# Performance work log

Measured on AMD Instinct MI355X. Metric: run time of the kernel, lower is better.

## Reference

```python
import jax, jax.numpy as jnp
import numpy as np

EMBED_DIM = 1024
NUM_HEADS = 16
HEAD_DIM = EMBED_DIM // NUM_HEADS


def setup_inputs() -> dict:
    key = jax.random.key(0)
    k1, k2, k3 = jax.random.split(key, 3)
    B, S = 2, 2048
    scale_in = 1.0 / np.sqrt(EMBED_DIM)
    x = jax.random.normal(k1, (B, S, EMBED_DIM), dtype=jnp.float32)
    Wqkv = jax.random.normal(k2, (EMBED_DIM, 3 * EMBED_DIM), dtype=jnp.float32) * scale_in
    bqkv = jnp.zeros((3 * EMBED_DIM,), dtype=jnp.float32)
    Wout = jax.random.normal(k3, (EMBED_DIM, EMBED_DIM), dtype=jnp.float32) * scale_in
    bout = jnp.zeros((EMBED_DIM,), dtype=jnp.float32)
    return {"x": x, "Wqkv": Wqkv, "bqkv": bqkv, "Wout": Wout, "bout": bout}


def reference(x, Wqkv, bqkv, Wout, bout):
    # Causal multi-head self-attention (dropout in eval mode = identity).
    B, S, E = x.shape
    qkv = x @ Wqkv + bqkv                                  # [B,S,3E]
    qkv = qkv.reshape(B, S, 3, NUM_HEADS, HEAD_DIM)
    qkv = jnp.transpose(qkv, (2, 0, 3, 1, 4))              # [3,B,H,S,D]
    q, k, v = qkv[0], qkv[1], qkv[2]
    scores = jnp.einsum("bhqd,bhkd->bhqk", q, k) / np.sqrt(HEAD_DIM)
    causal = jnp.tril(jnp.ones((S, S), dtype=bool))
    scores = jnp.where(causal, scores, -jnp.inf)
    attn = jax.nn.softmax(scores, axis=-1)                 # [B,H,S,S]
    out = jnp.einsum("bhqk,bhkd->bhqd", attn, v)           # [B,H,S,D]
    out = jnp.transpose(out, (0, 2, 1, 3)).reshape(B, S, E)
    return out @ Wout + bout
```

## Files before the change

### kernel.cpp

```cpp
#include <hip/hip_runtime.h>
#include <hip/hip_bf16.h>

#define BB 2
#define SS 2048
#define EE 1024
#define HH 16
#define DD 64
#define MT (BB*SS)
#define NQ (3*EE)

typedef unsigned short u16;
typedef __bf16 bf16t;
typedef bf16t bf16x8 __attribute__((ext_vector_type(8)));
typedef short short8v __attribute__((ext_vector_type(8)));
typedef float f32x4 __attribute__((ext_vector_type(4)));

#define AS1 __attribute__((address_space(1)))
#define AS3 __attribute__((address_space(3)))

__device__ __forceinline__ u16 f2b(float f) {
  unsigned u = __builtin_bit_cast(unsigned, f);
  u += 0x7FFF + ((u >> 16) & 1);
  return (u16)(u >> 16);
}

__device__ __forceinline__ unsigned cvtpk(float lo, float hi) {
  unsigned r;
  asm("v_cvt_pk_bf16_f32 %0, %1, %2" : "=v"(r) : "v"(lo), "v"(hi));
  return r;
}

__device__ __forceinline__ void gload_lds16(const void* g, void* l) {
  __builtin_amdgcn_global_load_lds((const AS1 void*)(g), (AS3 void*)(l), 16, 0, 0);
}

__device__ __forceinline__ f32x4 mfma_bf16(short8v a, short8v b, f32x4 c) {
  return __builtin_amdgcn_mfma_f32_16x16x32_bf16(
      __builtin_bit_cast(bf16x8, a), __builtin_bit_cast(bf16x8, b), c, 0, 0, 0);
}

#define QSCALE 0.18033688f

__global__ void __launch_bounds__(256) cast_kernel(const float* __restrict__ in,
                                                   u16* __restrict__ out, int n) {
  int i = (blockIdx.x * 256 + threadIdx.x) * 4;
  if (i + 3 < n) {
    float4 v = *(const float4*)(in + i);
    ushort4 o;
    o.x = f2b(v.x); o.y = f2b(v.y); o.z = f2b(v.z); o.w = f2b(v.w);
    *(ushort4*)(out + i) = o;
  }
}

__global__ void __launch_bounds__(256) transpose_kernel(const float* __restrict__ W,
                                                        u16* __restrict__ WT,
                                                        int K, int N) {
  __shared__ float t[64][65];
  int k0 = blockIdx.y * 64, n0 = blockIdx.x * 64;
  int r = threadIdx.x >> 4;
  int c4 = (threadIdx.x & 15) * 4;
#pragma unroll
  for (int i = 0; i < 4; ++i) {
    float4 v = *(const float4*)(W + (size_t)(k0 + r + i * 16) * N + n0 + c4);
    t[r + i * 16][c4 + 0] = v.x; t[r + i * 16][c4 + 1] = v.y;
    t[r + i * 16][c4 + 2] = v.z; t[r + i * 16][c4 + 3] = v.w;
  }
  __syncthreads();
#pragma unroll
  for (int i = 0; i < 4; ++i) {
    ushort4 o;
    o.x = f2b(t[c4 + 0][r + i * 16]); o.y = f2b(t[c4 + 1][r + i * 16]);
    o.z = f2b(t[c4 + 2][r + i * 16]); o.w = f2b(t[c4 + 3][r + i * 16]);
    *(ushort4*)(WT + (size_t)(n0 + r + i * 16) * K + k0 + c4) = o;
  }
}

__global__ void __launch_bounds__(256) gemm_qkv_kernel(
    const u16* __restrict__ A, const u16* __restrict__ BT,
    const float* __restrict__ bias,
    u16* __restrict__ Qs, u16* __restrict__ Ks, u16* __restrict__ Vt) {
  __shared__ u16 As[8192];
  __shared__ u16 Bs[8192];
  const int K = EE;
  int tid = threadIdx.x;
  int w = tid >> 6, lane = tid & 63;
  int g = lane >> 4, q = lane & 15;
  int m0 = blockIdx.y * 128, n0 = blockIdx.x * 128;
  int wm = (w >> 1) * 64, wn = (w & 1) * 64;

  f32x4 acc[4][4] = {};

  int r = tid >> 2;
  int kc = (tid & 3) * 8;
  const u16* ga = A + (size_t)(m0 + r) * K + kc;
  const u16* gb = BT + (size_t)(n0 + r) * K + kc;
  u16* lA0 = As + w * 512;
  u16* lA1 = As + 2048 + w * 512;
  u16* lB0 = Bs + w * 512;
  u16* lB1 = Bs + 2048 + w * 512;

  gload_lds16(ga, lA0);
  gload_lds16(ga + 64 * K, lA1);
  gload_lds16(gb, lB0);
  gload_lds16(gb + 64 * K, lB1);
  ga += 32; gb += 32;
  __syncthreads();

  int cur = 0;
  for (int k0 = 0; k0 < K; k0 += 32) {
    if (k0 + 32 < K) {
      int nx = (cur ^ 1) * 4096;
      gload_lds16(ga, lA0 + nx);
      gload_lds16(ga + 64 * K, lA1 + nx);
      gload_lds16(gb, lB0 + nx);
      gload_lds16(gb + 64 * K, lB1 + nx);
      ga += 32; gb += 32;
    }
    const u16* Ab = As + cur * 4096;
    const u16* Bb = Bs + cur * 4096;
    short8v af[4], bfv[4];
#pragma unroll
    for (int m = 0; m < 4; ++m)
      af[m] = *(const short8v*)(Ab + (wm + m * 16 + q) * 32 + g * 8);
#pragma unroll
    for (int n = 0; n < 4; ++n)
      bfv[n] = *(const short8v*)(Bb + (wn + n * 16 + q) * 32 + g * 8);
#pragma unroll
    for (int m = 0; m < 4; ++m)
#pragma unroll
      for (int n = 0; n < 4; ++n)
        acc[m][n] = mfma_bf16(af[m], bfv[n], acc[m][n]);
    __syncthreads();
    cur ^= 1;
  }

#pragma unroll
  for (int m = 0; m < 4; ++m) {
    int row0 = m0 + wm + m * 16 + g * 4;
#pragma unroll
    for (int n = 0; n < 4; ++n) {
      int col = n0 + wn + n * 16 + q;
      float bi = bias[col];
      int t = col >> 10;
      int h = (col >> 6) & 15;
      int d = col & 63;
      int b = row0 >> 11, s0 = row0 & 2047;
      size_t bh = (size_t)b * HH + h;
      if (t == 2) {
        ushort4 vv;
        vv.x = f2b(acc[m][n][0] + bi); vv.y = f2b(acc[m][n][1] + bi);
        vv.z = f2b(acc[m][n][2] + bi); vv.w = f2b(acc[m][n][3] + bi);
        *(ushort4*)&Vt[(bh * DD + d) * SS + s0] = vv;
      } else if (t == 0) {
#pragma unroll
        for (int r2 = 0; r2 < 4; ++r2)
          Qs[(bh * SS + s0 + r2) * DD + d] = f2b((acc[m][n][r2] + bi) * QSCALE);
      } else {
#pragma unroll
        for (int r2 = 0; r2 < 4; ++r2)
          Ks[(bh * SS + s0 + r2) * DD + d] = f2b(acc[m][n][r2] + bi);
      }
    }
  }
}

__global__ void __launch_bounds__(1024) attn_kernel(
    const u16* __restrict__ Qg, const u16* __restrict__ Kg,
    const u16* __restrict__ Vg, u16* __restrict__ O) {
  __shared__ char lds[132096];
  const int tid = threadIdx.x;
  const int w = tid >> 6, lane = tid & 63;
  const int hv = w >> 3, ws = w & 7;
  const int g = lane >> 4, q = lane & 15;
  const int bid = blockIdx.x;
  const int bh = bid & 31;
  const int p = 15 - (bid >> 5);
  const int b = bh >> 4, h = bh & 15;
  char* Pw = lds + 98304 + w * 2048;
  const int qsw = (q & 7) << 4;

  const char* Qp = (const char*)Qg + (size_t)bh * (SS * 128);
  const char* Kp = (const char*)Kg + (size_t)bh * (SS * 128);
  const char* Vp = (const char*)Vg + (size_t)bh * (SS * 128);

  const int tl = tid & 511;
  const int srow = tl >> 3;
  const int ssw = ((tl & 7) * 16) ^ ((srow & 7) << 4);
  const char* Ksrc = Kp + srow * 128 + ssw;
  const char* Vsrc = Vp + (size_t)srow * (SS * 2) + ssw;
  char* Kdst = lds + hv * 24576 + ws * 1024;
  char* Vdst = lds + 49152 + hv * 24576 + ws * 1024;

  const int hl = p + 1;
  const int s0 = hv * hl, send = s0 + hl;
  const int qw = p * 128 + ws * 16;

  short8v aq0 = *(const short8v*)(Qp + (size_t)(qw + q) * 128 + g * 16);
  short8v aq1 = *(const short8v*)(Qp + (size_t)(qw + q) * 128 + 64 + g * 16);

  f32x4 oacc[4] = {};
  float mrun = -1e30f, lrun = 0.f;

  gload_lds16(Ksrc + (size_t)s0 * 8192, Kdst);
  gload_lds16(Vsrc + s0 * 128, Vdst);
  if (hl > 1) {
    gload_lds16(Ksrc + (size_t)(s0 + 1) * 8192, Kdst + 8192);
    gload_lds16(Vsrc + (s0 + 1) * 128, Vdst + 8192);
  }

  for (int s = s0; s < send; ++s) {
    const int buf = (s - s0) % 3;
    if (s + 1 < send) asm volatile("s_waitcnt vmcnt(2)" ::: "memory");
    else              asm volatile("s_waitcnt vmcnt(0)" ::: "memory");
    __builtin_amdgcn_s_barrier();
    if (s + 2 < send) {
      int nb = (s + 2 - s0) % 3;
      gload_lds16(Ksrc + (size_t)(s + 2) * 8192, Kdst + nb * 8192);
      gload_lds16(Vsrc + (s + 2) * 128, Vdst + nb * 8192);
    }
    const int kv0 = s << 6;
    if (kv0 <= qw + 15) {
      const char* Kc = lds + hv * 24576 + buf * 8192;
      const char* Vc = lds + 49152 + hv * 24576 + buf * 8192;
      short8v kf[4][2];
#pragma unroll
      for (int cc = 0; cc < 4; ++cc) {
        const char* kb = Kc + (cc * 16 + q) * 128;
        kf[cc][0] = *(const short8v*)(kb + ((g * 16) ^ qsw));
        kf[cc][1] = *(const short8v*)(kb + ((64 + g * 16) ^ qsw));
      }
      f32x4 st[4];
      __builtin_amdgcn_s_setprio(1);
#pragma unroll
      for (int cc = 0; cc < 4; ++cc) {
        f32x4 z = {};
        z = mfma_bf16(kf[cc][0], aq0, z);
        z = mfma_bf16(kf[cc][1], aq1, z);
        st[cc] = z;
      }
      __builtin_amdgcn_s_setprio(0);
      short8v vf[4][2];
#pragma unroll
      for (int v = 0; v < 4; ++v) {
        const char* vb = Vc + (v * 16 + q) * 128;
        vf[v][0] = *(const short8v*)(vb + ((g * 16) ^ qsw));
        vf[v][1] = *(const short8v*)(vb + ((64 + g * 16) ^ qsw));
      }
      if (kv0 + 63 > qw) {
        int row = qw + q;
#pragma unroll
        for (int cc = 0; cc < 4; ++cc) {
          int kvb = kv0 + cc * 16 + g * 4;
#pragma unroll
          for (int r2 = 0; r2 < 4; ++r2)
            if (kvb + r2 > row) st[cc][r2] = -1e30f;
        }
      }
      f32x4 t01, t23;
#pragma unroll
      for (int r2 = 0; r2 < 4; ++r2) {
        t01[r2] = fmaxf(st[0][r2], st[1][r2]);
        t23[r2] = fmaxf(st[2][r2], st[3][r2]);
      }
      float mx = fmaxf(fmaxf(fmaxf(t01[0], t01[1]), fmaxf(t01[2], t01[3])),
                       fmaxf(fmaxf(t23[0], t23[1]), fmaxf(t23[2], t23[3])));
      mx = fmaxf(mx, __shfl_xor(mx, 16));
      mx = fmaxf(mx, __shfl_xor(mx, 32));
      if (!__all(mx - mrun <= 8.f)) {
        float mnew = fmaxf(mrun, mx);
        float alpha = exp2f(mrun - mnew);
        mrun = mnew;
        lrun *= alpha;
#pragma unroll
        for (int vfi = 0; vfi < 4; ++vfi)
#pragma unroll
          for (int r2 = 0; r2 < 4; ++r2) oacc[vfi][r2] *= alpha;
      }
      f32x4 sum4 = {};
#pragma unroll
      for (int cc = 0; cc < 4; ++cc)
#pragma unroll
        for (int r2 = 0; r2 < 4; ++r2) {
          float pv = exp2f(st[cc][r2] - mrun);
          st[cc][r2] = pv;
          sum4[r2] += pv;
        }
      float sm = (sum4[0] + sum4[1]) + (sum4[2] + sum4[3]);
      sm += __shfl_xor(sm, 16);
      sm += __shfl_xor(sm, 32);
      lrun += sm;
      char* basep = Pw + q * 128;
#pragma unroll
      for (int cc = 0; cc < 4; ++cc) {
        unsigned p01 = cvtpk(st[cc][0], st[cc][1]);
        unsigned p23 = cvtpk(st[cc][2], st[cc][3]);
        *(unsigned*)(basep + ((32 * cc + 8 * g + 0) ^ qsw)) = p01;
        *(unsigned*)(basep + ((32 * cc + 8 * g + 4) ^ qsw)) = p23;
      }
      short8v pa0 = *(const short8v*)(basep + ((g * 16) ^ qsw));
      short8v pa1 = *(const short8v*)(basep + ((64 + g * 16) ^ qsw));
      __builtin_amdgcn_s_setprio(1);
#pragma unroll
      for (int vfi = 0; vfi < 4; ++vfi) {
        oacc[vfi] = mfma_bf16(vf[vfi][0], pa0, oacc[vfi]);
        oacc[vfi] = mfma_bf16(vf[vfi][1], pa1, oacc[vfi]);
      }
      __builtin_amdgcn_s_setprio(0);
    }
  }

  __syncthreads();
  if (hv) {
    char* ob = lds + 98304 + ws * 4096;
#pragma unroll
    for (int vfi = 0; vfi < 4; ++vfi)
      *(f32x4*)(ob + vfi * 1024 + lane * 16) = oacc[vfi];
    if (g == 0)
      *(float2*)(lds + 131072 + (ws * 16 + q) * 8) = make_float2(mrun, lrun);
  }
  __syncthreads();
  if (!hv) {
    float2 ml = *(const float2*)(lds + 131072 + (ws * 16 + q) * 8);
    float mf = fmaxf(mrun, ml.x);
    float a0 = exp2f(mrun - mf);
    float a1 = exp2f(ml.x - mf);
    float inv = 1.0f / (a0 * lrun + a1 * ml.y);
    a0 *= inv; a1 *= inv;
    const char* ob = lds + 98304 + ws * 4096;
    int row = qw + q;
    char* obase = (char*)O + (((size_t)b * SS + row) * EE + h * 64) * 2;
#pragma unroll
    for (int vfi = 0; vfi < 4; ++vfi) {
      f32x4 o1 = *(const f32x4*)(ob + vfi * 1024 + lane * 16);
      uint2 o;
      o.x = cvtpk(a0 * oacc[vfi][0] + a1 * o1[0],
                  a0 * oacc[vfi][1] + a1 * o1[1]);
      o.y = cvtpk(a0 * oacc[vfi][2] + a1 * o1[2],
                  a0 * oacc[vfi][3] + a1 * o1[3]);
      *(uint2*)(obase + (vfi * 16 + g * 4) * 2) = o;
    }
  }
}

__global__ void __launch_bounds__(256) gemm_out_kernel(
    const u16* __restrict__ A, const u16* __restrict__ BT,
    const float* __restrict__ bias, float* __restrict__ Cout) {
  __shared__ u16 As[8192];
  __shared__ u16 Bs[8192];
  const int K = EE;
  int tid = threadIdx.x;
  int w = tid >> 6, lane = tid & 63;
  int g = lane >> 4, q = lane & 15;
  int m0 = blockIdx.y * 128, n0 = blockIdx.x * 128;
  int wm = (w >> 1) * 64, wn = (w & 1) * 64;

  f32x4 acc[4][4] = {};

  int r = tid >> 2;
  int kc = (tid & 3) * 8;
  const u16* ga = A + (size_t)(m0 + r) * K + kc;
  const u16* gb = BT + (size_t)(n0 + r) * K + kc;
  u16* lA0 = As + w * 512;
  u16* lA1 = As + 2048 + w * 512;
  u16* lB0 = Bs + w * 512;
  u16* lB1 = Bs + 2048 + w * 512;

  gload_lds16(ga, lA0);
  gload_lds16(ga + 64 * K, lA1);
  gload_lds16(gb, lB0);
  gload_lds16(gb + 64 * K, lB1);
  ga += 32; gb += 32;
  __syncthreads();

  int cur = 0;
  for (int k0 = 0; k0 < K; k0 += 32) {
    if (k0 + 32 < K) {
      int nx = (cur ^ 1) * 4096;
      gload_lds16(ga, lA0 + nx);
      gload_lds16(ga + 64 * K, lA1 + nx);
      gload_lds16(gb, lB0 + nx);
      gload_lds16(gb + 64 * K, lB1 + nx);
      ga += 32; gb += 32;
    }
    const u16* Ab = As + cur * 4096;
    const u16* Bb = Bs + cur * 4096;
    short8v af[4], bfv[4];
#pragma unroll
    for (int m = 0; m < 4; ++m)
      af[m] = *(const short8v*)(Ab + (wm + m * 16 + q) * 32 + g * 8);
#pragma unroll
    for (int n = 0; n < 4; ++n)
      bfv[n] = *(const short8v*)(Bb + (wn + n * 16 + q) * 32 + g * 8);
#pragma unroll
    for (int m = 0; m < 4; ++m)
#pragma unroll
      for (int n = 0; n < 4; ++n)
        acc[m][n] = mfma_bf16(af[m], bfv[n], acc[m][n]);
    __syncthreads();
    cur ^= 1;
  }

#pragma unroll
  for (int m = 0; m < 4; ++m) {
    int row0 = m0 + wm + m * 16 + g * 4;
#pragma unroll
    for (int n = 0; n < 4; ++n) {
      int col = n0 + wn + n * 16 + q;
      float bi = bias[col];
#pragma unroll
      for (int r2 = 0; r2 < 4; ++r2) {
        int row = row0 + r2;
        Cout[(size_t)row * EE + col] = acc[m][n][r2] + bi;
      }
    }
  }
}

extern "C" void kernel_launch(void* const* d_in, const int* in_sizes, int n_in,
                              void* d_out, int out_size, void* d_ws, size_t ws_size,
                              hipStream_t stream) {
  (void)in_sizes; (void)n_in; (void)out_size; (void)ws_size;
  const float* x    = (const float*)d_in[0];
  const float* Wqkv = (const float*)d_in[1];
  const float* bqkv = (const float*)d_in[2];
  const float* Wout = (const float*)d_in[3];
  const float* bout = (const float*)d_in[4];
  float* out = (float*)d_out;

  char* p = (char*)d_ws;
  u16* xb  = (u16*)p; p += (size_t)MT * EE * 2;
  u16* wqT = (u16*)p; p += (size_t)NQ * EE * 2;
  u16* woT = (u16*)p; p += (size_t)EE * EE * 2;
  u16* Qs  = (u16*)p; p += (size_t)BB * HH * SS * DD * 2;
  u16* Ks  = (u16*)p; p += (size_t)BB * HH * SS * DD * 2;
  u16* Vt  = (u16*)p; p += (size_t)BB * HH * DD * SS * 2;
  u16* Ob  = (u16*)p; p += (size_t)MT * EE * 2;

  cast_kernel<<<dim3((MT * EE / 4) / 256), dim3(256), 0, stream>>>(x, xb, MT * EE);
  transpose_kernel<<<dim3(NQ / 64, EE / 64), dim3(256), 0, stream>>>(Wqkv, wqT, EE, NQ);
  transpose_kernel<<<dim3(EE / 64, EE / 64), dim3(256), 0, stream>>>(Wout, woT, EE, EE);
  gemm_qkv_kernel<<<dim3(NQ / 128, MT / 128), dim3(256), 0, stream>>>(xb, wqT, bqkv, Qs, Ks, Vt);
  attn_kernel<<<dim3(512), dim3(1024), 0, stream>>>(Qs, Ks, Vt, Ob);
  gemm_out_kernel<<<dim3(EE / 128, MT / 128), dim3(256), 0, stream>>>(Ob, woT, bout, out);
}
```

Baseline: 116.6 us.

## Pass softmax P through lane shuffles and switch KV pipeline to double buffering

The attention kernel no longer stages the bf16 probability tile through per-wave LDS scratch. It builds the MFMA A-operand with cross-lane shuffles and selects instead. The K/V prefetch also moves from a three-stage ring with explicit vmcnt waits to a two-buffer scheme with a full __syncthreads each iteration. Together these cut LDS use from about 129 KB to 64 KB, but the per-iteration block barrier serializes the load of the next tile with compute more tightly. The 16 shuffles per iteration add cross-lane traffic in place of the LDS writes and reads.

```diff
diff --git a/kernel.cpp b/kernel.cpp
--- a/kernel.cpp
+++ b/kernel.cpp
@@ -14,6 +14,7 @@
 typedef bf16t bf16x8 __attribute__((ext_vector_type(8)));
 typedef short short8v __attribute__((ext_vector_type(8)));
 typedef float f32x4 __attribute__((ext_vector_type(4)));
+typedef unsigned uint4v __attribute__((ext_vector_type(4)));
 
 #define AS1 __attribute__((address_space(1)))
 #define AS3 __attribute__((address_space(3)))
@@ -167,7 +168,7 @@
 __global__ void __launch_bounds__(1024) attn_kernel(
     const u16* __restrict__ Qg, const u16* __restrict__ Kg,
     const u16* __restrict__ Vg, u16* __restrict__ O) {
-  __shared__ char lds[132096];
+  __shared__ char lds[65536];
   const int tid = threadIdx.x;
   const int w = tid >> 6, lane = tid & 63;
   const int hv = w >> 3, ws = w & 7;
@@ -176,7 +177,6 @@
   const int bh = bid & 31;
   const int p = 15 - (bid >> 5);
   const int b = bh >> 4, h = bh & 15;
-  char* Pw = lds + 98304 + w * 2048;
   const int qsw = (q & 7) << 4;
 
   const char* Qp = (const char*)Qg + (size_t)bh * (SS * 128);
@@ -188,11 +188,11 @@
   const int ssw = ((tl & 7) * 16) ^ ((srow & 7) << 4);
   const char* Ksrc = Kp + srow * 128 + ssw;
   const char* Vsrc = Vp + (size_t)srow * (SS * 2) + ssw;
-  char* Kdst = lds + hv * 24576 + ws * 1024;
-  char* Vdst = lds + 49152 + hv * 24576 + ws * 1024;
+  char* Kdst = lds + hv * 16384 + ws * 1024;
+  char* Vdst = lds + 32768 + hv * 16384 + ws * 1024;
 
   const int hl = p + 1;
-  const int s0 = hv * hl, send = s0 + hl;
+  const int s0 = hv * hl;
   const int qw = p * 128 + ws * 16;
 
   short8v aq0 = *(const short8v*)(Qp + (size_t)(qw + q) * 128 + g * 16);
@@ -201,27 +201,25 @@
   f32x4 oacc[4] = {};
   float mrun = -1e30f, lrun = 0.f;
 
+  const int srcA = 32 * (g & 1) + q;
+  const int srcB = srcA + 16;
+  const bool hi = (g & 2) != 0;
+
   gload_lds16(Ksrc + (size_t)s0 * 8192, Kdst);
   gload_lds16(Vsrc + s0 * 128, Vdst);
-  if (hl > 1) {
-    gload_lds16(Ksrc + (size_t)(s0 + 1) * 8192, Kdst + 8192);
-    gload_lds16(Vsrc + (s0 + 1) * 128, Vdst + 8192);
-  }
-
-  for (int s = s0; s < send; ++s) {
-    const int buf = (s - s0) % 3;
-    if (s + 1 < send) asm volatile("s_waitcnt vmcnt(2)" ::: "memory");
-    else              asm volatile("s_waitcnt vmcnt(0)" ::: "memory");
-    __builtin_amdgcn_s_barrier();
-    if (s + 2 < send) {
-      int nb = (s + 2 - s0) % 3;
-      gload_lds16(Ksrc + (size_t)(s + 2) * 8192, Kdst + nb * 8192);
-      gload_lds16(Vsrc + (s + 2) * 128, Vdst + nb * 8192);
+  __syncthreads();
+
+  for (int ls = 0; ls < hl; ++ls) {
+    const int s = s0 + ls;
+    const int buf = ls & 1;
+    if (ls + 1 < hl) {
+      gload_lds16(Ksrc + (size_t)(s + 1) * 8192, Kdst + (buf ^ 1) * 8192);
+      gload_lds16(Vsrc + (s + 1) * 128, Vdst + (buf ^ 1) * 8192);
     }
     const int kv0 = s << 6;
     if (kv0 <= qw + 15) {
-      const char* Kc = lds + hv * 24576 + buf * 8192;
-      const char* Vc = lds + 49152 + hv * 24576 + buf * 8192;
+      const char* Kc = lds + hv * 16384 + buf * 8192;
+      const char* Vc = lds + 32768 + hv * 16384 + buf * 8192;
       short8v kf[4][2];
 #pragma unroll
       for (int cc = 0; cc < 4; ++cc) {
@@ -289,16 +287,34 @@
       sm += __shfl_xor(sm, 16);
       sm += __shfl_xor(sm, 32);
       lrun += sm;
-      char* basep = Pw + q * 128;
+      unsigned p01[4], p23[4];
 #pragma unroll
       for (int cc = 0; cc < 4; ++cc) {
-        unsigned p01 = cvtpk(st[cc][0], st[cc][1]);
-        unsigned p23 = cvtpk(st[cc][2], st[cc][3]);
-        *(unsigned*)(basep + ((32 * cc + 8 * g + 0) ^ qsw)) = p01;
-        *(unsigned*)(basep + ((32 * cc + 8 * g + 4) ^ qsw)) = p23;
-      }
-      short8v pa0 = *(const short8v*)(basep + ((g * 16) ^ qsw));
-      short8v pa1 = *(const short8v*)(basep + ((64 + g * 16) ^ qsw));
+        p01[cc] = cvtpk(st[cc][0], st[cc][1]);
+        p23[cc] = cvtpk(st[cc][2], st[cc][3]);
+      }
+      uint4v pa0u, pa1u;
+      {
+        unsigned t0, t1;
+        t0 = __shfl((int)p01[0], srcA); t1 = __shfl((int)p01[1], srcA);
+        pa0u[0] = hi ? t1 : t0;
+        t0 = __shfl((int)p23[0], srcA); t1 = __shfl((int)p23[1], srcA);
+        pa0u[1] = hi ? t1 : t0;
+        t0 = __shfl((int)p01[0], srcB); t1 = __shfl((int)p01[1], srcB);
+        pa0u[2] = hi ? t1 : t0;
+        t0 = __shfl((int)p23[0], srcB); t1 = __shfl((int)p23[1], srcB);
+        pa0u[3] = hi ? t1 : t0;
+        t0 = __shfl((int)p01[2], srcA); t1 = __shfl((int)p01[3], srcA);
+        pa1u[0] = hi ? t1 : t0;
+        t0 = __shfl((int)p23[2], srcA); t1 = __shfl((int)p23[3], srcA);
+        pa1u[1] = hi ? t1 : t0;
+        t0 = __shfl((int)p01[2], srcB); t1 = __shfl((int)p01[3], srcB);
+        pa1u[2] = hi ? t1 : t0;
+        t0 = __shfl((int)p23[2], srcB); t1 = __shfl((int)p23[3], srcB);
+        pa1u[3] = hi ? t1 : t0;
+      }
+      short8v pa0 = __builtin_bit_cast(short8v, pa0u);
+      short8v pa1 = __builtin_bit_cast(short8v, pa1u);
       __builtin_amdgcn_s_setprio(1);
 #pragma unroll
       for (int vfi = 0; vfi < 4; ++vfi) {
@@ -307,26 +323,26 @@
       }
       __builtin_amdgcn_s_setprio(0);
     }
-  }
-
-  __syncthreads();
+    __syncthreads();
+  }
+
   if (hv) {
-    char* ob = lds + 98304 + ws * 4096;
+    char* ob = lds + ws * 4096;
 #pragma unroll
     for (int vfi = 0; vfi < 4; ++vfi)
       *(f32x4*)(ob + vfi * 1024 + lane * 16) = oacc[vfi];
     if (g == 0)
-      *(float2*)(lds + 131072 + (ws * 16 + q) * 8) = make_float2(mrun, lrun);
+      *(float2*)(lds + 32768 + (ws * 16 + q) * 8) = make_float2(mrun, lrun);
   }
   __syncthreads();
   if (!hv) {
-    float2 ml = *(const float2*)(lds + 131072 + (ws * 16 + q) * 8);
+    float2 ml = *(const float2*)(lds + 32768 + (ws * 16 + q) * 8);
     float mf = fmaxf(mrun, ml.x);
     float a0 = exp2f(mrun - mf);
     float a1 = exp2f(ml.x - mf);
     float inv = 1.0f / (a0 * lrun + a1 * ml.y);
     a0 *= inv; a1 *= inv;
-    const char* ob = lds + 98304 + ws * 4096;
+    const char* ob = lds + ws * 4096;
     int row = qw + q;
     char* obase = (char*)O + (((size_t)b * SS + row) * EE + h * 64) * 2;
 #pragma unroll
```

Measured after the change: 117.4 us. Within noise of the previous version (+0.7%).

## Merge weight transposes into one launch and remap GEMM blocks per XCD

Applied to the files above, without the earlier changes.

Combines the two weight transpose launches into a single kernel that picks its matrix from the block index, removing one launch. The QKV GEMM grid becomes 1D and is remapped so each of the 8 XCDs (bid&7) owns a contiguous group of 3 N-tiles, which should improve L2 reuse of weight tiles within each die. The output GEMM also moves to a 1D grid with row-major tile order. The extra index arithmetic is negligible, though the XCD mapping assumes round-robin dispatch of blocks across dies.

```diff
diff --git a/kernel.cpp b/kernel.cpp
--- a/kernel.cpp
+++ b/kernel.cpp
@@ -52,11 +52,16 @@
   }
 }
 
-__global__ void __launch_bounds__(256) transpose_kernel(const float* __restrict__ W,
-                                                        u16* __restrict__ WT,
-                                                        int K, int N) {
+__global__ void __launch_bounds__(256) transpose2_kernel(
+    const float* __restrict__ Wq, u16* __restrict__ WqT,
+    const float* __restrict__ Wo, u16* __restrict__ WoT) {
   __shared__ float t[64][65];
-  int k0 = blockIdx.y * 64, n0 = blockIdx.x * 64;
+  int bid = blockIdx.x;
+  const float* W; u16* WT; int N, xt, yt;
+  if (bid < 768) { W = Wq; WT = WqT; N = NQ; xt = bid % 48; yt = bid / 48; }
+  else { int b2 = bid - 768; W = Wo; WT = WoT; N = EE; xt = b2 & 15; yt = b2 >> 4; }
+  const int K = EE;
+  int k0 = yt * 64, n0 = xt * 64;
   int r = threadIdx.x >> 4;
   int c4 = (threadIdx.x & 15) * 4;
 #pragma unroll
@@ -85,7 +90,11 @@
   int tid = threadIdx.x;
   int w = tid >> 6, lane = tid & 63;
   int g = lane >> 4, q = lane & 15;
-  int m0 = blockIdx.y * 128, n0 = blockIdx.x * 128;
+  int bid = blockIdx.x;
+  int xcd = bid & 7, idx = bid >> 3;
+  int xt = xcd * 3 + (idx % 3);
+  int yt = idx / 3;
+  int m0 = yt * 128, n0 = xt * 128;
   int wm = (w >> 1) * 64, wn = (w & 1) * 64;
 
   f32x4 acc[4][4] = {};
@@ -351,7 +360,9 @@
   int tid = threadIdx.x;
   int w = tid >> 6, lane = tid & 63;
   int g = lane >> 4, q = lane & 15;
-  int m0 = blockIdx.y * 128, n0 = blockIdx.x * 128;
+  int bid = blockIdx.x;
+  int xt = bid & 7, yt = bid >> 3;
+  int m0 = yt * 128, n0 = xt * 128;
   int wm = (w >> 1) * 64, wn = (w & 1) * 64;
 
   f32x4 acc[4][4] = {};
@@ -437,9 +448,8 @@
   u16* Ob  = (u16*)p; p += (size_t)MT * EE * 2;
 
   cast_kernel<<<dim3((MT * EE / 4) / 256), dim3(256), 0, stream>>>(x, xb, MT * EE);
-  transpose_kernel<<<dim3(NQ / 64, EE / 64), dim3(256), 0, stream>>>(Wqkv, wqT, EE, NQ);
-  transpose_kernel<<<dim3(EE / 64, EE / 64), dim3(256), 0, stream>>>(Wout, woT, EE, EE);
-  gemm_qkv_kernel<<<dim3(NQ / 128, MT / 128), dim3(256), 0, stream>>>(xb, wqT, bqkv, Qs, Ks, Vt);
+  transpose2_kernel<<<dim3(1024), dim3(256), 0, stream>>>(Wqkv, wqT, Wout, woT);
+  gemm_qkv_kernel<<<dim3(768), dim3(256), 0, stream>>>(xb, wqT, bqkv, Qs, Ks, Vt);
   attn_kernel<<<dim3(512), dim3(1024), 0, stream>>>(Qs, Ks, Vt, Ob);
-  gemm_out_kernel<<<dim3(EE / 128, MT / 128), dim3(256), 0, stream>>>(Ob, woT, bout, out);
-}
+  gemm_out_kernel<<<dim3(256), dim3(256), 0, stream>>>(Ob, woT, bout, out);
+}
```

Result: no change. 115.1 us, median of 3 (-1.3%).
